# Kernel optimization log

Measured on AMD Instinct MI355X. Metric: run time of the kernel, lower is better.

The kernel has to match this reference:

```python
import jax, jax.numpy as jnp
import numpy as np

N_NODES = 100000
N_EDGES = 600000
D_IN = 128
HID = 128
N_LAYERS = 3


def gcn_conv(x, W, b, src, dst, num_nodes):
    """PyG-style GCNConv: D^{-1/2}(A+I)D^{-1/2} X W + b (self-loops added)."""
    h = x @ W  # [N, H]
    # in-degree including self-loop
    deg = jnp.zeros((num_nodes,), dtype=x.dtype).at[dst].add(1.0) + 1.0
    dinv = jax.lax.rsqrt(deg)
    norm = dinv[src] * dinv[dst]  # [E]
    msg = h[src] * norm[:, None]  # [E, H] gather + scale
    out = jax.ops.segment_sum(msg, dst, num_segments=num_nodes)  # scatter-add
    out = out + h * (1.0 / deg)[:, None]  # self-loop term (norm = 1/deg)
    return out + b


def setup_inputs() -> dict:
    key = jax.random.key(0)
    ks = jax.random.split(key, 16)
    x = jax.random.normal(ks[0], (N_NODES, D_IN), dtype=jnp.float32)
    edge_index = jax.random.randint(ks[1], (2, N_EDGES), 0, N_NODES, dtype=jnp.int64)
    timestamp = jax.random.uniform(ks[2], (1,), dtype=jnp.float32)
    # GCN layer weights (glorot-ish scale) and biases
    def glorot(k, fan_in, fan_out):
        s = jnp.sqrt(6.0 / (fan_in + fan_out))
        return jax.random.uniform(k, (fan_in, fan_out), minval=-s, maxval=s, dtype=jnp.float32)
    W_gcn = [glorot(ks[3], D_IN, HID), glorot(ks[4], HID, HID), glorot(ks[5], HID, HID)]
    b_gcn = [jnp.zeros((HID,), jnp.float32) for _ in range(N_LAYERS)]
    # temporal gate MLP: Linear(1,H) -> tanh -> Linear(H,H) -> sigmoid
    Wg1 = glorot(ks[6], 1, HID)
    bg1 = jnp.zeros((HID,), jnp.float32)
    Wg2 = glorot(ks[7], HID, HID)
    bg2 = jnp.zeros((HID,), jnp.float32)
    return {
        "x": x, "edge_index": edge_index, "timestamp": timestamp,
        "W0": W_gcn[0], "b0": b_gcn[0],
        "W1": W_gcn[1], "b1": b_gcn[1],
        "W2": W_gcn[2], "b2": b_gcn[2],
        "Wg1": Wg1, "bg1": bg1, "Wg2": Wg2, "bg2": bg2,
    }


def reference(x, edge_index, timestamp, W0, b0, W1, b1, W2, b2, Wg1, bg1, Wg2, bg2):
    src, dst = edge_index[0], edge_index[1]
    num_nodes = x.shape[0]
    # temporal gate: [1,1] -> [1,H], broadcast over nodes
    t = timestamp.reshape(1, 1)
    gate = jax.nn.sigmoid(jnp.tanh(t @ Wg1 + bg1) @ Wg2 + bg2)  # [1, H]
    for (W, b) in ((W0, b0), (W1, b1), (W2, b2)):
        x = gcn_conv(x, W, b, src, dst, num_nodes)
        x = jax.nn.relu(x)
        x = x * gate  # broadcast gate over nodes
        # dropout: identity in eval mode
    return x
```

## Files before the change

### kernel.cpp

```cpp
#include <hip/hip_runtime.h>
#include <hip/hip_bf16.h>
#include <hip/hip_fp16.h>
#include <math.h>


#define D 128

typedef __attribute__((ext_vector_type(8))) short short8;
typedef __attribute__((ext_vector_type(8))) _Float16 half8;
typedef __attribute__((ext_vector_type(4))) float floatx4;

__device__ __forceinline__ unsigned bf16_rne(float x) {
    unsigned u = __float_as_uint(x);
    return (u + 0x7FFFu + ((u >> 16) & 1u)) >> 16;
}

__device__ __forceinline__ void gload_lds16(const void* g, void* l) {
    __builtin_amdgcn_global_load_lds(
        (const __attribute__((address_space(1))) unsigned int*)g,
        (__attribute__((address_space(3))) unsigned int*)l, 16, 0, 0);
}

__device__ __forceinline__ float h2f(unsigned short u) {
    return __half2float(__ushort_as_half(u));
}

__global__ __launch_bounds__(256) void prep_kernel(
    const int* __restrict__ w, int* __restrict__ src32,
    int* __restrict__ dst32, int* __restrict__ counts, int E,
    const float* __restrict__ W0, const float* __restrict__ W1,
    const float* __restrict__ W2, short8* __restrict__ Wf_hi,
    short8* __restrict__ Wf_lo,
    const float* __restrict__ t, const float* __restrict__ Wg1,
    const float* __restrict__ bg1, const float* __restrict__ Wg2,
    const float* __restrict__ bg2, float* __restrict__ gate)
{
    int b = blockIdx.x;
    if (b < 24) {
        int f = b * 256 + threadIdx.x;
        int layer = f >> 11;
        int fi = f & 2047;
        int lane = fi & 63;
        int tt = fi >> 6;
        int kc = tt >> 3, n = tt & 7;
        const float* W = (layer == 0) ? W0 : (layer == 1) ? W1 : W2;
        int krow = kc * 32 + (lane >> 4) * 8;
        int col = n * 16 + (lane & 15);
        short8 hv, lv;
        if (layer == 0) {
            #pragma unroll
            for (int j = 0; j < 8; j++) {
                float x = W[(size_t)(krow + j) * D + col];
                unsigned hb = bf16_rne(x);
                float hf = __uint_as_float(hb << 16);
                unsigned lb = bf16_rne(x - hf);
                hv[j] = (short)hb;
                lv[j] = (short)lb;
            }
        } else {
            #pragma unroll
            for (int j = 0; j < 8; j++) {
                float x = W[(size_t)(krow + j) * D + col];
                __half hh = __float2half(x);
                float hf = __half2float(hh);
                __half ll = __float2half(x - hf);
                hv[j] = (short)__half_as_ushort(hh);
                lv[j] = (short)__half_as_ushort(ll);
            }
        }
        Wf_hi[f] = hv;
        Wf_lo[f] = lv;
        return;
    }
    if (b == 24) {
        __shared__ float u[D];
        int j = threadIdx.x;
        if (j < D) {
            float tv = t[0];
            u[j] = tanhf(tv * Wg1[j] + bg1[j]);
        }
        __syncthreads();
        if (j < D) {
            float s = bg2[j];
            #pragma unroll 8
            for (int k = 0; k < D; k++) s += u[k] * Wg2[k * D + j];
            gate[j] = 1.0f / (1.0f + expf(-s));
        }
        return;
    }
    __shared__ int flag;
    if (threadIdx.x == 0) {
        int z = 0;
        for (int k = 0; k < 64; k++) z |= w[2 * k + 1];
        flag = (z == 0) ? 1 : 0;
    }
    __syncthreads();
    int i64 = flag;
    int e = (b - 25) * 256 + threadIdx.x;
    if (e >= E) return;
    int s = i64 ? w[2 * e] : w[e];
    int d = i64 ? w[2 * (E + e)] : w[E + e];
    src32[e] = s;
    dst32[e] = d;
    atomicAdd(&counts[d], 1);
}

#define SCHUNK 1024
#define RBITS 8
#define RSZ 256
__device__ __forceinline__ int cap4(int c) { return (c + 3) & ~3; }

__global__ __launch_bounds__(256) void scan_partial_kernel(
    const int* __restrict__ counts, int* __restrict__ bsums, int N)
{
    int base = blockIdx.x * SCHUNK + threadIdx.x * 4;
    int s = 0;
    if (base + 3 < N) {
        int4 v = *(const int4*)(counts + base);
        s = cap4(v.x) + cap4(v.y) + cap4(v.z) + cap4(v.w);
    } else {
        for (int k = 0; k < 4; k++) if (base + k < N) s += cap4(counts[base + k]);
    }
    #pragma unroll
    for (int off = 1; off < 64; off <<= 1) s += __shfl_xor(s, off);
    __shared__ int wsum[4];
    int lane = threadIdx.x & 63, wid = threadIdx.x >> 6;
    if (lane == 0) wsum[wid] = s;
    __syncthreads();
    if (threadIdx.x == 0)
        bsums[blockIdx.x] = wsum[0] + wsum[1] + wsum[2] + wsum[3];
}

__global__ __launch_bounds__(1024) void scan_bsums_kernel(
    int* __restrict__ bsums, int* __restrict__ total_out, int B)
{
    int t = threadIdx.x;
    int v = (t < B) ? bsums[t] : 0;
    int lane = t & 63, wid = t >> 6;
    int s = v;
    #pragma unroll
    for (int off = 1; off < 64; off <<= 1) {
        int n = __shfl_up(s, off);
        if (lane >= off) s += n;
    }
    __shared__ int wsum[16], wpre[16];
    if (lane == 63) wsum[wid] = s;
    __syncthreads();
    if (t < 16) {
        int ws = wsum[t];
        #pragma unroll
        for (int off = 1; off < 16; off <<= 1) {
            int n = __shfl_up(ws, off);
            if (t >= off) ws += n;
        }
        wpre[t] = ws;
    }
    __syncthreads();
    int wex = wid ? wpre[wid - 1] : 0;
    if (t < B) bsums[t] = wex + (s - v);
    if (t == 0) *total_out = wpre[15];
}

__global__ __launch_bounds__(256) void scan_final_kernel(
    const int* __restrict__ counts, const int* __restrict__ bsums,
    int* __restrict__ offsets, int* __restrict__ cursor2,
    float* __restrict__ dinv, int N)
{
    int base = blockIdx.x * SCHUNK + threadIdx.x * 4;
    int c[4];
    float dd[4];
    bool full = (base + 3 < N);
    if (full) {
        int4 v = *(const int4*)(counts + base);
        c[0] = cap4(v.x); c[1] = cap4(v.y); c[2] = cap4(v.z); c[3] = cap4(v.w);
        dd[0] = rsqrtf((float)(v.x + 1)); dd[1] = rsqrtf((float)(v.y + 1));
        dd[2] = rsqrtf((float)(v.z + 1)); dd[3] = rsqrtf((float)(v.w + 1));
    } else {
        for (int k = 0; k < 4; k++) {
            int r = (base + k < N) ? counts[base + k] : 0;
            c[k] = (base + k < N) ? cap4(r) : 0;
            dd[k] = rsqrtf((float)(r + 1));
        }
    }
    int sum = c[0] + c[1] + c[2] + c[3];
    int lane = threadIdx.x & 63, wid = threadIdx.x >> 6;
    int s = sum;
    #pragma unroll
    for (int off = 1; off < 64; off <<= 1) {
        int n = __shfl_up(s, off);
        if (lane >= off) s += n;
    }
    __shared__ int wsum[4], wpre[4];
    if (lane == 63) wsum[wid] = s;
    __syncthreads();
    if (threadIdx.x == 0) {
        int a = 0;
        #pragma unroll
        for (int k = 0; k < 4; k++) { wpre[k] = a; a += wsum[k]; }
    }
    __syncthreads();
    int e0 = bsums[blockIdx.x] + wpre[wid] + (s - sum);
    int4 o = make_int4(e0, e0 + c[0], e0 + c[0] + c[1], e0 + c[0] + c[1] + c[2]);
    float4 dv = make_float4(dd[0], dd[1], dd[2], dd[3]);
    if (full) {
        *(int4*)(offsets + base) = o;
        *(float4*)(dinv + base) = dv;
    } else {
        int oo[4] = { o.x, o.y, o.z, o.w };
        for (int k = 0; k < 4; k++)
            if (base + k < N) {
                offsets[base + k] = oo[k];
                dinv[base + k] = dd[k];
            }
    }
    if ((base & (RSZ - 1)) == 0 && base < N) cursor2[base >> RBITS] = e0;
}

#define P1E 16
__global__ __launch_bounds__(256) void binpass_kernel(
    const int* __restrict__ src32, const int* __restrict__ dst32,
    int* __restrict__ cursor2, int2* __restrict__ stag, int E, int B)
{
    __shared__ int cnt[512];
    __shared__ int base[512];
    int tid = threadIdx.x;
    for (int i = tid; i < B; i += 256) cnt[i] = 0;
    __syncthreads();
    int e0 = blockIdx.x * (P1E * 256) + tid;
    int s[P1E], d[P1E], lp[P1E];
    #pragma unroll
    for (int k = 0; k < P1E; k++) {
        int e = e0 + k * 256;
        if (e < E) {
            s[k] = src32[e];
            d[k] = dst32[e];
            lp[k] = atomicAdd(&cnt[d[k] >> RBITS], 1);
        }
    }
    __syncthreads();
    for (int i = tid; i < B; i += 256)
        base[i] = cnt[i] ? atomicAdd(&cursor2[i], cnt[i]) : 0;
    __syncthreads();
    #pragma unroll
    for (int k = 0; k < P1E; k++) {
        int e = e0 + k * 256;
        if (e < E)
            stag[base[d[k] >> RBITS] + lp[k]] = make_int2(s[k], d[k]);
    }
}

#define P2CAP 4096
__global__ __launch_bounds__(256) void place_kernel(
    const int2* __restrict__ stag, const int* __restrict__ cursor2,
    const int* __restrict__ offsets, const float* __restrict__ dinv,
    int2* __restrict__ edges8, int N)
{
    __shared__ int2 buf[P2CAP];
    __shared__ int loff[RSZ + 1];
    __shared__ int lcnt[RSZ];
    int b = blockIdx.x;
    int tid = threadIdx.x;
    int d0 = b * RSZ;
    int d1 = (d0 + RSZ < N) ? d0 + RSZ : N;
    int nd = d1 - d0;
    for (int i = tid; i <= nd; i += 256) loff[i] = offsets[d0 + i];
    for (int i = tid; i < nd; i += 256) lcnt[i] = 0;
    __syncthreads();
    int regionStart = loff[0];
    int regionSize = loff[nd] - regionStart;
    int ecount = cursor2[b] - regionStart;
    if (regionSize <= P2CAP) {
        for (int i = tid; i < regionSize; i += 256) buf[i] = make_int2(0, 0);
        __syncthreads();
        for (int i = tid; i < ecount; i += 256) {
            int2 sd = stag[regionStart + i];
            int ld = sd.y - d0;
            int pos = loff[ld] - regionStart + atomicAdd(&lcnt[ld], 1);
            buf[pos] = make_int2(sd.x, __float_as_int(dinv[sd.x]));
        }
        __syncthreads();
        for (int i = tid; i < regionSize; i += 256)
            edges8[regionStart + i] = buf[i];
    } else {
        for (int i = tid; i < regionSize; i += 256)
            edges8[regionStart + i] = make_int2(0, 0);
        __syncthreads();
        for (int i = tid; i < ecount; i += 256) {
            int2 sd = stag[regionStart + i];
            int ld = sd.y - d0;
            int pos = loff[ld] + atomicAdd(&lcnt[ld], 1);
            edges8[pos] = make_int2(sd.x, __float_as_int(dinv[sd.x]));
        }
    }
}

#define WSTAGE(kc_)                                                           \
    {                                                                         \
        short* wb_ = Wfs + (((kc_) & 1) ? 8192 : 0);                          \
        const short8* gh_ = Wf_hi + (size_t)(kc_) * 512;                      \
        const short8* gl_ = Wf_lo + (size_t)(kc_) * 512;                      \
        _Pragma("unroll")                                                     \
        for (int i_ = 0; i_ < 2; i_++) {                                      \
            int c_ = i_ * 256 + w * 64;                                       \
            gload_lds16(gh_ + c_ + lane, wb_ + c_ * 8);                       \
            gload_lds16(gl_ + c_ + lane, wb_ + 4096 + c_ * 8);                \
        }                                                                     \
    }

#define MFMA_BLOCK(kc)                                                        \
    {                                                                         \
        const short* wb = Wfs + (((kc) & 1) ? 8192 : 0);                      \
        _Pragma("unroll")                                                     \
        for (int n = 0; n < 8; n++) {                                         \
            short8 bh = *(const short8*)(wb + (n * 64 + lane) * 8);           \
            short8 bl = *(const short8*)(wb + 4096 + (n * 64 + lane) * 8);    \
            acc[0][n] = __builtin_amdgcn_mfma_f32_16x16x32_bf16(ah0, bh, acc[0][n], 0, 0, 0); \
            acc[0][n] = __builtin_amdgcn_mfma_f32_16x16x32_bf16(ah0, bl, acc[0][n], 0, 0, 0); \
            acc[0][n] = __builtin_amdgcn_mfma_f32_16x16x32_bf16(al0, bh, acc[0][n], 0, 0, 0); \
            acc[1][n] = __builtin_amdgcn_mfma_f32_16x16x32_bf16(ah1, bh, acc[1][n], 0, 0, 0); \
            acc[1][n] = __builtin_amdgcn_mfma_f32_16x16x32_bf16(ah1, bl, acc[1][n], 0, 0, 0); \
            acc[1][n] = __builtin_amdgcn_mfma_f32_16x16x32_bf16(al1, bh, acc[1][n], 0, 0, 0); \
        }                                                                     \
    }

#define MFMA_BLOCK_F16(kc)                                                    \
    {                                                                         \
        const short* wb = Wfs + (((kc) & 1) ? 8192 : 0);                      \
        _Pragma("unroll")                                                     \
        for (int n = 0; n < 8; n++) {                                         \
            half8 bh = *(const half8*)(wb + (n * 64 + lane) * 8);             \
            half8 bl = *(const half8*)(wb + 4096 + (n * 64 + lane) * 8);      \
            acc[0][n] = __builtin_amdgcn_mfma_f32_16x16x32_f16(ah0, bh, acc[0][n], 0, 0, 0); \
            acc[0][n] = __builtin_amdgcn_mfma_f32_16x16x32_f16(ah0, bl, acc[0][n], 0, 0, 0); \
            acc[1][n] = __builtin_amdgcn_mfma_f32_16x16x32_f16(ah1, bh, acc[1][n], 0, 0, 0); \
            acc[1][n] = __builtin_amdgcn_mfma_f32_16x16x32_f16(ah1, bl, acc[1][n], 0, 0, 0); \
        }                                                                     \
    }

#define EPILOGUE()                                                            \
    _Pragma("unroll")                                                         \
    for (int rt = 0; rt < 2; rt++) {                                          \
        _Pragma("unroll")                                                     \
        for (int reg = 0; reg < 4; reg++) {                                   \
            int row = rowbase + rt * 16 + qd * 4 + reg;                       \
            if (row < M) {                                                    \
                unsigned short* hp = H16 + (size_t)row * D + m16;             \
                _Pragma("unroll")                                             \
                for (int n = 0; n < 8; n++)                                   \
                    hp[n * 16] = __half_as_ushort(__float2half(acc[rt][n][reg])); \
            }                                                                 \
        }                                                                     \
    }

#define GBM 128
__device__ __forceinline__ void cvt8(const float* f, short8& hi, short8& lo) {
    #pragma unroll
    for (int j = 0; j < 8; j++) {
        unsigned hb = bf16_rne(f[j]);
        float hf = __uint_as_float(hb << 16);
        unsigned lb = bf16_rne(f[j] - hf);
        hi[j] = (short)hb;
        lo[j] = (short)lb;
    }
}

__global__ __launch_bounds__(256) void gemm_f32_kernel(
    const float* __restrict__ X, const short8* __restrict__ Wf_hi,
    const short8* __restrict__ Wf_lo, unsigned short* __restrict__ H16, int M)
{
    __shared__ short Wfs[16384];
    int tid = threadIdx.x;
    int w = tid >> 6, lane = tid & 63;
    int m16 = lane & 15, qd = lane >> 4;
    int rowbase = blockIdx.x * GBM + w * 32;

    int r0 = rowbase + m16;      if (r0 >= M) r0 = M - 1;
    int r1 = rowbase + m16 + 16; if (r1 >= M) r1 = M - 1;
    const float* xp0 = X + (size_t)r0 * D + qd * 8;
    const float* xp1 = X + (size_t)r1 * D + qd * 8;

    floatx4 acc[2][8];
    #pragma unroll
    for (int rt = 0; rt < 2; rt++)
        #pragma unroll
        for (int n = 0; n < 8; n++)
            acc[rt][n] = (floatx4)(0.f);

    #define LOADA(kc_, A0, A1)                                              \
        {                                                                   \
            *(float4*)(A0)     = *(const float4*)(xp0 + (kc_) * 32);        \
            *(float4*)(A0 + 4) = *(const float4*)(xp0 + (kc_) * 32 + 4);    \
            *(float4*)(A1)     = *(const float4*)(xp1 + (kc_) * 32);        \
            *(float4*)(A1 + 4) = *(const float4*)(xp1 + (kc_) * 32 + 4);    \
        }

    float a0c[8], a1c[8], a0n[8], a1n[8];
    WSTAGE(0)
    LOADA(0, a0c, a1c)

    #pragma unroll
    for (int kc = 0; kc < 4; kc++) {
        __syncthreads();
        if (kc < 3) {
            WSTAGE(kc + 1)
            LOADA(kc + 1, a0n, a1n)
        }
        short8 ah0, al0, ah1, al1;
        cvt8(a0c, ah0, al0);
        cvt8(a1c, ah1, al1);
        MFMA_BLOCK(kc)
        if (kc < 3) {
            #pragma unroll
            for (int z = 0; z < 8; z++) { a0c[z] = a0n[z]; a1c[z] = a1n[z]; }
        }
    }
    #undef LOADA
    EPILOGUE()
}

__global__ __launch_bounds__(256) void gemm_f16_kernel(
    const unsigned short* __restrict__ Xh,
    const short8* __restrict__ Wf_hi, const short8* __restrict__ Wf_lo,
    unsigned short* __restrict__ H16, int M)
{
    __shared__ short Wfs[16384];
    int tid = threadIdx.x;
    int w = tid >> 6, lane = tid & 63;
    int m16 = lane & 15, qd = lane >> 4;
    int rowbase = blockIdx.x * GBM + w * 32;

    int r0 = rowbase + m16;      if (r0 >= M) r0 = M - 1;
    int r1 = rowbase + m16 + 16; if (r1 >= M) r1 = M - 1;
    const unsigned short* xh0 = Xh + (size_t)r0 * D + qd * 8;
    const unsigned short* xh1 = Xh + (size_t)r1 * D + qd * 8;

    floatx4 acc[2][8];
    #pragma unroll
    for (int rt = 0; rt < 2; rt++)
        #pragma unroll
        for (int n = 0; n < 8; n++)
            acc[rt][n] = (floatx4)(0.f);

    half8 ah0, ah1, nh0, nh1;
    WSTAGE(0)
    ah0 = *(const half8*)(xh0);
    ah1 = *(const half8*)(xh1);

    #pragma unroll
    for (int kc = 0; kc < 4; kc++) {
        __syncthreads();
        if (kc < 3) {
            WSTAGE(kc + 1)
            nh0 = *(const half8*)(xh0 + (kc + 1) * 32);
            nh1 = *(const half8*)(xh1 + (kc + 1) * 32);
        }
        MFMA_BLOCK_F16(kc)
        if (kc < 3) { ah0 = nh0; ah1 = nh1; }
    }
    EPILOGUE()
}

__global__ __launch_bounds__(256) void agg_kernel(
    const unsigned short* __restrict__ H16, const int2* __restrict__ edges,
    const int* __restrict__ offsets, const float* __restrict__ dinv,
    const float* __restrict__ bias, const float* __restrict__ gate,
    float* __restrict__ outF, unsigned short* __restrict__ outH,
    int M, int writeF32)
{
    int t = threadIdx.x;
    int hw = t >> 5;
    int l32 = t & 31;
    int node = blockIdx.x * 8 + hw;
    if (node >= M) return;

    int beg = offsets[node];
    int end = offsets[node + 1];
    float dv = dinv[node];
    const unsigned short* __restrict__ Hc = H16 + l32 * 4;
    ushort4 us = *(const ushort4*)(Hc + (size_t)node * D);
    float4 acc = make_float4(0.f, 0.f, 0.f, 0.f);

    if (beg < end) {
        int4 p0 = *(const int4*)(edges + beg);
        int4 p1 = *(const int4*)(edges + beg + 2);
        ushort4 u0 = *(const ushort4*)(Hc + (size_t)p0.x * D);
        ushort4 u1 = *(const ushort4*)(Hc + (size_t)p0.z * D);
        ushort4 u2 = *(const ushort4*)(Hc + (size_t)p1.x * D);
        ushort4 u3 = *(const ushort4*)(Hc + (size_t)p1.z * D);
        int j1 = (beg + 4 < end) ? beg + 4 : beg;
        int4 q0 = *(const int4*)(edges + j1);
        int4 q1 = *(const int4*)(edges + j1 + 2);

        for (int j = beg; j < end; j += 4) {
            int jn = j + 8;
            int jp = (jn < end) ? jn : beg;
            int4 r0 = *(const int4*)(edges + jp);
            int4 r1 = *(const int4*)(edges + jp + 2);
            ushort4 v0 = *(const ushort4*)(Hc + (size_t)q0.x * D);
            ushort4 v1 = *(const ushort4*)(Hc + (size_t)q0.z * D);
            ushort4 v2 = *(const ushort4*)(Hc + (size_t)q1.x * D);
            ushort4 v3 = *(const ushort4*)(Hc + (size_t)q1.z * D);
            float n0 = __int_as_float(p0.y) * dv, n1 = __int_as_float(p0.w) * dv;
            float n2 = __int_as_float(p1.y) * dv, n3 = __int_as_float(p1.w) * dv;
            acc.x = fmaf(h2f(u3.x), n3, fmaf(h2f(u2.x), n2, fmaf(h2f(u1.x), n1, fmaf(h2f(u0.x), n0, acc.x))));
            acc.y = fmaf(h2f(u3.y), n3, fmaf(h2f(u2.y), n2, fmaf(h2f(u1.y), n1, fmaf(h2f(u0.y), n0, acc.y))));
            acc.z = fmaf(h2f(u3.z), n3, fmaf(h2f(u2.z), n2, fmaf(h2f(u1.z), n1, fmaf(h2f(u0.z), n0, acc.z))));
            acc.w = fmaf(h2f(u3.w), n3, fmaf(h2f(u2.w), n2, fmaf(h2f(u1.w), n1, fmaf(h2f(u0.w), n0, acc.w))));
            p0 = q0; p1 = q1; q0 = r0; q1 = r1;
            u0 = v0; u1 = v1; u2 = v2; u3 = v3;
        }
    }

    float nself = dv * dv;
    acc.x = fmaf(h2f(us.x), nself, acc.x);
    acc.y = fmaf(h2f(us.y), nself, acc.y);
    acc.z = fmaf(h2f(us.z), nself, acc.z);
    acc.w = fmaf(h2f(us.w), nself, acc.w);

    float4 bv = *(const float4*)(bias + l32 * 4);
    float4 gv = *(const float4*)(gate + l32 * 4);
    acc.x = fmaxf(acc.x + bv.x, 0.f) * gv.x;
    acc.y = fmaxf(acc.y + bv.y, 0.f) * gv.y;
    acc.z = fmaxf(acc.z + bv.z, 0.f) * gv.z;
    acc.w = fmaxf(acc.w + bv.w, 0.f) * gv.w;

    if (writeF32) {
        *(float4*)(outF + (size_t)node * D + l32 * 4) = acc;
    } else {
        ushort4 hs = make_ushort4(
            __half_as_ushort(__float2half(acc.x)),
            __half_as_ushort(__float2half(acc.y)),
            __half_as_ushort(__float2half(acc.z)),
            __half_as_ushort(__float2half(acc.w)));
        *(ushort4*)(outH + (size_t)node * D + l32 * 4) = hs;
    }
}

static inline size_t align_up(size_t v, size_t a) { return (v + a - 1) & ~(a - 1); }

extern "C" void kernel_launch(void* const* d_in, const int* in_sizes, int n_in,
                              void* d_out, int out_size, void* d_ws, size_t ws_size,
                              hipStream_t stream)
{
    const float* x   = (const float*)d_in[0];
    const int*   ei  = (const int*)d_in[1];
    const float* ts  = (const float*)d_in[2];
    const float* Wl[3] = { (const float*)d_in[3], (const float*)d_in[5], (const float*)d_in[7] };
    const float* bl[3] = { (const float*)d_in[4], (const float*)d_in[6], (const float*)d_in[8] };
    const float* Wg1 = (const float*)d_in[9];
    const float* bg1 = (const float*)d_in[10];
    const float* Wg2 = (const float*)d_in[11];
    const float* bg2 = (const float*)d_in[12];

    const int N = in_sizes[0] / D;
    const int E = in_sizes[1] / 2;
    const int NB = (N + SCHUNK - 1) / SCHUNK;
    const int B  = (N + RSZ - 1) / RSZ;
    const size_t ECAP = (size_t)E + 3 * (size_t)N;

    char* p = (char*)d_ws;
    unsigned short* h16 = (unsigned short*)p; p += align_up((size_t)N * D * 2, 256);
    unsigned short* xh  = (unsigned short*)p; p += align_up((size_t)N * D * 2, 256);
    int* src32  = (int*)p;   p += align_up((size_t)E * 4, 256);
    int* dst32  = (int*)p;   p += align_up((size_t)E * 4, 256);
    int* counts = (int*)p;   p += align_up((size_t)N * 4, 256);
    float* dinv = (float*)p; p += align_up((size_t)N * 4, 256);
    int* offs   = (int*)p;   p += align_up((size_t)(N + 1) * 4, 256);
    int* cursor2 = (int*)p;  p += align_up((size_t)B * 4, 256);
    int2* stag  = (int2*)p;  p += align_up(ECAP * 8, 256);
    int2* edges8 = (int2*)p; p += align_up(ECAP * 8, 256);
    float* gate = (float*)p; p += align_up((size_t)D * 4, 256);
    int* bsums  = (int*)p;   p += align_up((size_t)NB * 4, 256);
    short8* Wf_hi = (short8*)p; p += align_up((size_t)3 * 2048 * 16, 256);
    short8* Wf_lo = (short8*)p; p += align_up((size_t)3 * 2048 * 16, 256);
    (void)ws_size; (void)n_in; (void)out_size;

    (void)hipMemsetAsync(counts, 0, (size_t)N * 4, stream);

    int egrid = (E + 255) / 256;
    prep_kernel<<<25 + egrid, 256, 0, stream>>>(
        ei, src32, dst32, counts, E,
        Wl[0], Wl[1], Wl[2], Wf_hi, Wf_lo,
        ts, Wg1, bg1, Wg2, bg2, gate);
    scan_partial_kernel<<<NB, 256, 0, stream>>>(counts, bsums, N);
    scan_bsums_kernel<<<1, 1024, 0, stream>>>(bsums, offs + N, NB);
    scan_final_kernel<<<NB, 256, 0, stream>>>(counts, bsums, offs, cursor2, dinv, N);
    int g1 = (E + P1E * 256 - 1) / (P1E * 256);
    binpass_kernel<<<g1, 256, 0, stream>>>(src32, dst32, cursor2, stag, E, B);
    place_kernel<<<B, 256, 0, stream>>>(stag, cursor2, offs, dinv, edges8, N);

    int ggrid = (N + GBM - 1) / GBM;
    int agrid = (N + 7) / 8;
    gemm_f32_kernel<<<ggrid, 256, 0, stream>>>(x, Wf_hi, Wf_lo, h16, N);
    agg_kernel<<<agrid, 256, 0, stream>>>(h16, edges8, offs, dinv, bl[0], gate,
                                          nullptr, xh, N, 0);
    gemm_f16_kernel<<<ggrid, 256, 0, stream>>>(xh, Wf_hi + 2048, Wf_lo + 2048, h16, N);
    agg_kernel<<<agrid, 256, 0, stream>>>(h16, edges8, offs, dinv, bl[1], gate,
                                          nullptr, xh, N, 0);
    gemm_f16_kernel<<<ggrid, 256, 0, stream>>>(xh, Wf_hi + 4096, Wf_lo + 4096, h16, N);
    agg_kernel<<<agrid, 256, 0, stream>>>(h16, edges8, offs, dinv, bl[2], gate,
                                          (float*)d_out, nullptr, N, 1);
}
```

Before: 226.9 us.

## Replace global degree scan with fixed-capacity per-bin CSR buckets

Removes the global atomic degree count, memset and three-kernel prefix scan. Each 256-node bin instead gets a fixed-capacity slot region in the staging and edge buffers. A new place1 kernel counts degrees per bin in shared memory and does a local scan to build begin/end offsets and dinv, and place2 scatters edges into the padded bin. This cuts several small serialized launches and the global atomics, at the cost of assuming no bin exceeds 4096 edges and of sparser edge arrays read by the aggregation kernels.

```diff
diff --git a/kernel.cpp b/kernel.cpp
--- a/kernel.cpp
+++ b/kernel.cpp
@@ -10,6 +10,11 @@
 typedef __attribute__((ext_vector_type(8))) _Float16 half8;
 typedef __attribute__((ext_vector_type(4))) float floatx4;
 
+#define RBITS 8
+#define RSZ 256
+#define SCAP 4096
+#define RCAP 4096
+
 __device__ __forceinline__ unsigned bf16_rne(float x) {
     unsigned u = __float_as_uint(x);
     return (u + 0x7FFFu + ((u >> 16) & 1u)) >> 16;
@@ -25,15 +30,18 @@
     return __half2float(__ushort_as_half(u));
 }
 
+__device__ __forceinline__ int cap4(int c) { return (c + 3) & ~3; }
+
 __global__ __launch_bounds__(256) void prep_kernel(
     const int* __restrict__ w, int* __restrict__ src32,
-    int* __restrict__ dst32, int* __restrict__ counts, int E,
+    int* __restrict__ dst32, int E,
     const float* __restrict__ W0, const float* __restrict__ W1,
     const float* __restrict__ W2, short8* __restrict__ Wf_hi,
     short8* __restrict__ Wf_lo,
     const float* __restrict__ t, const float* __restrict__ Wg1,
     const float* __restrict__ bg1, const float* __restrict__ Wg2,
-    const float* __restrict__ bg2, float* __restrict__ gate)
+    const float* __restrict__ bg2, float* __restrict__ gate,
+    int* __restrict__ cursor2, int B)
 {
     int b = blockIdx.x;
     if (b < 24) {
@@ -73,6 +81,7 @@
         return;
     }
     if (b == 24) {
+        for (int i = threadIdx.x; i < B; i += 256) cursor2[i] = i * SCAP;
         __shared__ float u[D];
         int j = threadIdx.x;
         if (j < D) {
@@ -102,118 +111,6 @@
     int d = i64 ? w[2 * (E + e)] : w[E + e];
     src32[e] = s;
     dst32[e] = d;
-    atomicAdd(&counts[d], 1);
-}
-
-#define SCHUNK 1024
-#define RBITS 8
-#define RSZ 256
-__device__ __forceinline__ int cap4(int c) { return (c + 3) & ~3; }
-
-__global__ __launch_bounds__(256) void scan_partial_kernel(
-    const int* __restrict__ counts, int* __restrict__ bsums, int N)
-{
-    int base = blockIdx.x * SCHUNK + threadIdx.x * 4;
-    int s = 0;
-    if (base + 3 < N) {
-        int4 v = *(const int4*)(counts + base);
-        s = cap4(v.x) + cap4(v.y) + cap4(v.z) + cap4(v.w);
-    } else {
-        for (int k = 0; k < 4; k++) if (base + k < N) s += cap4(counts[base + k]);
-    }
-    #pragma unroll
-    for (int off = 1; off < 64; off <<= 1) s += __shfl_xor(s, off);
-    __shared__ int wsum[4];
-    int lane = threadIdx.x & 63, wid = threadIdx.x >> 6;
-    if (lane == 0) wsum[wid] = s;
-    __syncthreads();
-    if (threadIdx.x == 0)
-        bsums[blockIdx.x] = wsum[0] + wsum[1] + wsum[2] + wsum[3];
-}
-
-__global__ __launch_bounds__(1024) void scan_bsums_kernel(
-    int* __restrict__ bsums, int* __restrict__ total_out, int B)
-{
-    int t = threadIdx.x;
-    int v = (t < B) ? bsums[t] : 0;
-    int lane = t & 63, wid = t >> 6;
-    int s = v;
-    #pragma unroll
-    for (int off = 1; off < 64; off <<= 1) {
-        int n = __shfl_up(s, off);
-        if (lane >= off) s += n;
-    }
-    __shared__ int wsum[16], wpre[16];
-    if (lane == 63) wsum[wid] = s;
-    __syncthreads();
-    if (t < 16) {
-        int ws = wsum[t];
-        #pragma unroll
-        for (int off = 1; off < 16; off <<= 1) {
-            int n = __shfl_up(ws, off);
-            if (t >= off) ws += n;
-        }
-        wpre[t] = ws;
-    }
-    __syncthreads();
-    int wex = wid ? wpre[wid - 1] : 0;
-    if (t < B) bsums[t] = wex + (s - v);
-    if (t == 0) *total_out = wpre[15];
-}
-
-__global__ __launch_bounds__(256) void scan_final_kernel(
-    const int* __restrict__ counts, const int* __restrict__ bsums,
-    int* __restrict__ offsets, int* __restrict__ cursor2,
-    float* __restrict__ dinv, int N)
-{
-    int base = blockIdx.x * SCHUNK + threadIdx.x * 4;
-    int c[4];
-    float dd[4];
-    bool full = (base + 3 < N);
-    if (full) {
-        int4 v = *(const int4*)(counts + base);
-        c[0] = cap4(v.x); c[1] = cap4(v.y); c[2] = cap4(v.z); c[3] = cap4(v.w);
-        dd[0] = rsqrtf((float)(v.x + 1)); dd[1] = rsqrtf((float)(v.y + 1));
-        dd[2] = rsqrtf((float)(v.z + 1)); dd[3] = rsqrtf((float)(v.w + 1));
-    } else {
-        for (int k = 0; k < 4; k++) {
-            int r = (base + k < N) ? counts[base + k] : 0;
-            c[k] = (base + k < N) ? cap4(r) : 0;
-            dd[k] = rsqrtf((float)(r + 1));
-        }
-    }
-    int sum = c[0] + c[1] + c[2] + c[3];
-    int lane = threadIdx.x & 63, wid = threadIdx.x >> 6;
-    int s = sum;
-    #pragma unroll
-    for (int off = 1; off < 64; off <<= 1) {
-        int n = __shfl_up(s, off);
-        if (lane >= off) s += n;
-    }
-    __shared__ int wsum[4], wpre[4];
-    if (lane == 63) wsum[wid] = s;
-    __syncthreads();
-    if (threadIdx.x == 0) {
-        int a = 0;
-        #pragma unroll
-        for (int k = 0; k < 4; k++) { wpre[k] = a; a += wsum[k]; }
-    }
-    __syncthreads();
-    int e0 = bsums[blockIdx.x] + wpre[wid] + (s - sum);
-    int4 o = make_int4(e0, e0 + c[0], e0 + c[0] + c[1], e0 + c[0] + c[1] + c[2]);
-    float4 dv = make_float4(dd[0], dd[1], dd[2], dd[3]);
-    if (full) {
-        *(int4*)(offsets + base) = o;
-        *(float4*)(dinv + base) = dv;
-    } else {
-        int oo[4] = { o.x, o.y, o.z, o.w };
-        for (int k = 0; k < 4; k++)
-            if (base + k < N) {
-                offsets[base + k] = oo[k];
-                dinv[base + k] = dd[k];
-            }
-    }
-    if ((base & (RSZ - 1)) == 0 && base < N) cursor2[base >> RBITS] = e0;
 }
 
 #define P1E 16
@@ -244,52 +141,101 @@
     #pragma unroll
     for (int k = 0; k < P1E; k++) {
         int e = e0 + k * 256;
-        if (e < E)
-            stag[base[d[k] >> RBITS] + lp[k]] = make_int2(s[k], d[k]);
-    }
-}
-
-#define P2CAP 4096
-__global__ __launch_bounds__(256) void place_kernel(
+        if (e < E) {
+            int bin = d[k] >> RBITS;
+            int idx = base[bin] + lp[k];
+            if (idx < (bin + 1) * SCAP)
+                stag[idx] = make_int2(s[k], d[k]);
+        }
+    }
+}
+
+__global__ __launch_bounds__(256) void place1_kernel(
     const int2* __restrict__ stag, const int* __restrict__ cursor2,
-    const int* __restrict__ offsets, const float* __restrict__ dinv,
-    int2* __restrict__ edges8, int N)
-{
-    __shared__ int2 buf[P2CAP];
-    __shared__ int loff[RSZ + 1];
+    int* __restrict__ obeg, int* __restrict__ oend,
+    float* __restrict__ dinv, int N)
+{
+    __shared__ int cnt[RSZ];
+    __shared__ int wsum[4], wpre[4];
+    int b = blockIdx.x, tid = threadIdx.x;
+    int d0 = b * RSZ;
+    int nd = (d0 + RSZ < N) ? RSZ : N - d0;
+    cnt[tid] = 0;
+    __syncthreads();
+    int ecount = cursor2[b] - b * SCAP;
+    if (ecount > SCAP) ecount = SCAP;
+    const int2* sp = stag + (size_t)b * SCAP;
+    for (int i = tid; i < ecount; i += 256)
+        atomicAdd(&cnt[sp[i].y - d0], 1);
+    __syncthreads();
+    int c = (tid < nd) ? cnt[tid] : 0;
+    int cap = cap4(c);
+    int s = cap;
+    int lane = tid & 63, wid = tid >> 6;
+    #pragma unroll
+    for (int off = 1; off < 64; off <<= 1) {
+        int n = __shfl_up(s, off);
+        if (lane >= off) s += n;
+    }
+    if (lane == 63) wsum[wid] = s;
+    __syncthreads();
+    if (tid == 0) {
+        int a = 0;
+        #pragma unroll
+        for (int k = 0; k < 4; k++) { wpre[k] = a; a += wsum[k]; }
+    }
+    __syncthreads();
+    int pre = wpre[wid] + (s - cap);
+    if (tid < nd) {
+        int beg = b * RCAP + pre;
+        obeg[d0 + tid] = beg;
+        oend[d0 + tid] = beg + cap;
+        dinv[d0 + tid] = rsqrtf((float)(c + 1));
+    }
+}
+
+__global__ __launch_bounds__(256) void place2_kernel(
+    const int2* __restrict__ stag, const int* __restrict__ cursor2,
+    const int* __restrict__ obeg, const int* __restrict__ oend,
+    const float* __restrict__ dinv, int2* __restrict__ edges8, int N)
+{
+    __shared__ int2 buf[RCAP];
+    __shared__ int loff[RSZ];
     __shared__ int lcnt[RSZ];
-    int b = blockIdx.x;
-    int tid = threadIdx.x;
+    int b = blockIdx.x, tid = threadIdx.x;
     int d0 = b * RSZ;
-    int d1 = (d0 + RSZ < N) ? d0 + RSZ : N;
-    int nd = d1 - d0;
-    for (int i = tid; i <= nd; i += 256) loff[i] = offsets[d0 + i];
-    for (int i = tid; i < nd; i += 256) lcnt[i] = 0;
-    __syncthreads();
-    int regionStart = loff[0];
-    int regionSize = loff[nd] - regionStart;
-    int ecount = cursor2[b] - regionStart;
-    if (regionSize <= P2CAP) {
-        for (int i = tid; i < regionSize; i += 256) buf[i] = make_int2(0, 0);
+    int nd = (d0 + RSZ < N) ? RSZ : N - d0;
+    if (tid < nd) {
+        loff[tid] = obeg[d0 + tid] - b * RCAP;
+        lcnt[tid] = 0;
+    }
+    __syncthreads();
+    int totalcap = oend[d0 + nd - 1] - b * RCAP;
+    int ecount = cursor2[b] - b * SCAP;
+    if (ecount > SCAP) ecount = SCAP;
+    const int2* sp = stag + (size_t)b * SCAP;
+    int2* out = edges8 + (size_t)b * RCAP;
+    if (totalcap <= RCAP) {
+        for (int i = tid; i < totalcap; i += 256) buf[i] = make_int2(0, 0);
         __syncthreads();
         for (int i = tid; i < ecount; i += 256) {
-            int2 sd = stag[regionStart + i];
+            int2 sd = sp[i];
             int ld = sd.y - d0;
-            int pos = loff[ld] - regionStart + atomicAdd(&lcnt[ld], 1);
+            int pos = loff[ld] + atomicAdd(&lcnt[ld], 1);
             buf[pos] = make_int2(sd.x, __float_as_int(dinv[sd.x]));
         }
         __syncthreads();
-        for (int i = tid; i < regionSize; i += 256)
-            edges8[regionStart + i] = buf[i];
+        for (int i = tid; i < totalcap; i += 256) out[i] = buf[i];
     } else {
-        for (int i = tid; i < regionSize; i += 256)
-            edges8[regionStart + i] = make_int2(0, 0);
+        for (int i = tid; i < totalcap && i < RCAP; i += 256)
+            out[i] = make_int2(0, 0);
         __syncthreads();
         for (int i = tid; i < ecount; i += 256) {
-            int2 sd = stag[regionStart + i];
+            int2 sd = sp[i];
             int ld = sd.y - d0;
             int pos = loff[ld] + atomicAdd(&lcnt[ld], 1);
-            edges8[pos] = make_int2(sd.x, __float_as_int(dinv[sd.x]));
+            if (pos < RCAP)
+                out[pos] = make_int2(sd.x, __float_as_int(dinv[sd.x]));
         }
     }
 }
@@ -462,7 +408,8 @@
 
 __global__ __launch_bounds__(256) void agg_kernel(
     const unsigned short* __restrict__ H16, const int2* __restrict__ edges,
-    const int* __restrict__ offsets, const float* __restrict__ dinv,
+    const int* __restrict__ obeg, const int* __restrict__ oend,
+    const float* __restrict__ dinv,
     const float* __restrict__ bias, const float* __restrict__ gate,
     float* __restrict__ outF, unsigned short* __restrict__ outH,
     int M, int writeF32)
@@ -473,8 +420,8 @@
     int node = blockIdx.x * 8 + hw;
     if (node >= M) return;
 
-    int beg = offsets[node];
-    int end = offsets[node + 1];
+    int beg = obeg[node];
+    int end = oend[node];
     float dv = dinv[node];
     const unsigned short* __restrict__ Hc = H16 + l32 * 4;
     ushort4 us = *(const ushort4*)(Hc + (size_t)node * D);
@@ -554,50 +501,43 @@
 
     const int N = in_sizes[0] / D;
     const int E = in_sizes[1] / 2;
-    const int NB = (N + SCHUNK - 1) / SCHUNK;
-    const int B  = (N + RSZ - 1) / RSZ;
-    const size_t ECAP = (size_t)E + 3 * (size_t)N;
+    const int B = (N + RSZ - 1) / RSZ;
 
     char* p = (char*)d_ws;
     unsigned short* h16 = (unsigned short*)p; p += align_up((size_t)N * D * 2, 256);
     unsigned short* xh  = (unsigned short*)p; p += align_up((size_t)N * D * 2, 256);
     int* src32  = (int*)p;   p += align_up((size_t)E * 4, 256);
     int* dst32  = (int*)p;   p += align_up((size_t)E * 4, 256);
-    int* counts = (int*)p;   p += align_up((size_t)N * 4, 256);
     float* dinv = (float*)p; p += align_up((size_t)N * 4, 256);
-    int* offs   = (int*)p;   p += align_up((size_t)(N + 1) * 4, 256);
+    int* obeg   = (int*)p;   p += align_up((size_t)N * 4, 256);
+    int* oend   = (int*)p;   p += align_up((size_t)N * 4, 256);
     int* cursor2 = (int*)p;  p += align_up((size_t)B * 4, 256);
-    int2* stag  = (int2*)p;  p += align_up(ECAP * 8, 256);
-    int2* edges8 = (int2*)p; p += align_up(ECAP * 8, 256);
+    int2* stag  = (int2*)p;  p += align_up((size_t)B * SCAP * 8, 256);
+    int2* edges8 = (int2*)p; p += align_up((size_t)B * RCAP * 8, 256);
     float* gate = (float*)p; p += align_up((size_t)D * 4, 256);
-    int* bsums  = (int*)p;   p += align_up((size_t)NB * 4, 256);
     short8* Wf_hi = (short8*)p; p += align_up((size_t)3 * 2048 * 16, 256);
     short8* Wf_lo = (short8*)p; p += align_up((size_t)3 * 2048 * 16, 256);
     (void)ws_size; (void)n_in; (void)out_size;
 
-    (void)hipMemsetAsync(counts, 0, (size_t)N * 4, stream);
-
     int egrid = (E + 255) / 256;
     prep_kernel<<<25 + egrid, 256, 0, stream>>>(
-        ei, src32, dst32, counts, E,
+        ei, src32, dst32, E,
         Wl[0], Wl[1], Wl[2], Wf_hi, Wf_lo,
-        ts, Wg1, bg1, Wg2, bg2, gate);
-    scan_partial_kernel<<<NB, 256, 0, stream>>>(counts, bsums, N);
-    scan_bsums_kernel<<<1, 1024, 0, stream>>>(bsums, offs + N, NB);
-    scan_final_kernel<<<NB, 256, 0, stream>>>(counts, bsums, offs, cursor2, dinv, N);
+        ts, Wg1, bg1, Wg2, bg2, gate, cursor2, B);
     int g1 = (E + P1E * 256 - 1) / (P1E * 256);
     binpass_kernel<<<g1, 256, 0, stream>>>(src32, dst32, cursor2, stag, E, B);
-    place_kernel<<<B, 256, 0, stream>>>(stag, cursor2, offs, dinv, edges8, N);
+    place1_kernel<<<B, 256, 0, stream>>>(stag, cursor2, obeg, oend, dinv, N);
+    place2_kernel<<<B, 256, 0, stream>>>(stag, cursor2, obeg, oend, dinv, edges8, N);
 
     int ggrid = (N + GBM - 1) / GBM;
     int agrid = (N + 7) / 8;
     gemm_f32_kernel<<<ggrid, 256, 0, stream>>>(x, Wf_hi, Wf_lo, h16, N);
-    agg_kernel<<<agrid, 256, 0, stream>>>(h16, edges8, offs, dinv, bl[0], gate,
+    agg_kernel<<<agrid, 256, 0, stream>>>(h16, edges8, obeg, oend, dinv, bl[0], gate,
                                           nullptr, xh, N, 0);
     gemm_f16_kernel<<<ggrid, 256, 0, stream>>>(xh, Wf_hi + 2048, Wf_lo + 2048, h16, N);
-    agg_kernel<<<agrid, 256, 0, stream>>>(h16, edges8, offs, dinv, bl[1], gate,
+    agg_kernel<<<agrid, 256, 0, stream>>>(h16, edges8, obeg, oend, dinv, bl[1], gate,
                                           nullptr, xh, N, 0);
     gemm_f16_kernel<<<ggrid, 256, 0, stream>>>(xh, Wf_hi + 4096, Wf_lo + 4096, h16, N);
-    agg_kernel<<<agrid, 256, 0, stream>>>(h16, edges8, offs, dinv, bl[2], gate,
+    agg_kernel<<<agrid, 256, 0, stream>>>(h16, edges8, obeg, oend, dinv, bl[2], gate,
                                           (float*)d_out, nullptr, N, 1);
 }
```

Result: faster. 195.3 us (-13.9%).
